# Performance work log

Measured on AMD Instinct MI355X. Metric: run time of the kernel, lower is better.

Reference implementation:

```python
import jax, jax.numpy as jnp
import numpy as np
from jax import lax

B, Cin, C, H, W, Ns, K = 2, 64, 64, 256, 1216, 20000, 9
HW = H * W
D = 2 * C + 3   # 131, MLP input dim
Dh = D // 2     # 65, MLP hidden dim


def _conv(x, w, b, relu):
    y = lax.conv_general_dilated(x, w, (1, 1), 'SAME',
                                 dimension_numbers=('NCHW', 'OIHW', 'NCHW'))
    y = y + b[None, :, None, None]
    return jax.nn.relu(y) if relu else y


def _mlp(f, w1, b1, w2, b2):
    # f: (B, Ns, K, D) -> (B, Ns, K, 1)
    h = jax.nn.leaky_relu(f @ w1 + b1, 0.2)
    return h @ w2 + b2


def setup_inputs() -> dict:
    ks = jax.random.split(jax.random.key(0), 32)
    s = 0.05
    rng = np.random.default_rng(0)
    # unique point indices per batch (torch scatter with dup indices is nondeterministic)
    pc = np.stack([np.sort(rng.choice(HW, Ns, replace=False)) for _ in range(B)])[:, None, :]
    inp = {
        'rgb': jax.random.normal(ks[0], (B, Cin, H, W), jnp.float32),
        'sdepth': jax.random.normal(ks[1], (B, Cin, H, W), jnp.float32),
        'pc_idx': jnp.asarray(pc, dtype=jnp.int32),
        'nbrs_idx': jax.random.randint(ks[2], (B, 1, Ns, K), 0, HW, dtype=jnp.int32),
        'nbrs_disp': jax.random.normal(ks[3], (B, 3, Ns, K), jnp.float32),
        'd_conv0_w': jax.random.normal(ks[4], (C, Cin, 3, 3), jnp.float32) * s,
        'd_conv0_b': jnp.zeros((C,), jnp.float32),
        'd_conv1_w': jax.random.normal(ks[5], (C, Cin, 3, 3), jnp.float32) * s,
        'd_conv1_b': jnp.zeros((C,), jnp.float32),
        'd_conv2_w': jax.random.normal(ks[6], (C, C, 3, 3), jnp.float32) * s,
        'd_conv2_b': jnp.zeros((C,), jnp.float32),
        'r_conv0_w': jax.random.normal(ks[7], (C, Cin, 3, 3), jnp.float32) * s,
        'r_conv0_b': jnp.zeros((C,), jnp.float32),
        'r_conv1_w': jax.random.normal(ks[8], (C, Cin, 3, 3), jnp.float32) * s,
        'r_conv1_b': jnp.zeros((C,), jnp.float32),
        'r_conv2_w': jax.random.normal(ks[9], (C, C, 3, 3), jnp.float32) * s,
        'r_conv2_b': jnp.zeros((C,), jnp.float32),
        'd_w1': jax.random.normal(ks[10], (D, Dh), jnp.float32) * s,
        'd_b1': jnp.zeros((Dh,), jnp.float32),
        'd_w2': jax.random.normal(ks[11], (Dh, 1), jnp.float32) * s,
        'd_b2': jnp.zeros((1,), jnp.float32),
        'r_w1': jax.random.normal(ks[12], (D, Dh), jnp.float32) * s,
        'r_b1': jnp.zeros((Dh,), jnp.float32),
        'r_w2': jax.random.normal(ks[13], (Dh, 1), jnp.float32) * s,
        'r_b2': jnp.zeros((1,), jnp.float32),
        'd_bias': jnp.zeros((C,), jnp.float32),
        'r_bias': jnp.zeros((C,), jnp.float32),
    }
    return inp


def reference(rgb, sdepth, pc_idx, nbrs_idx, nbrs_disp,
              d_conv0_w, d_conv0_b, d_conv1_w, d_conv1_b, d_conv2_w, d_conv2_b,
              r_conv0_w, r_conv0_b, r_conv1_w, r_conv1_b, r_conv2_w, r_conv2_b,
              d_w1, d_b1, d_w2, d_b2, r_w1, r_b1, r_w2, r_b2, d_bias, r_bias):
    d0 = _conv(sdepth, d_conv0_w, d_conv0_b, True)
    d1 = _conv(sdepth, d_conv1_w, d_conv1_b, False)
    r0 = _conv(rgb, r_conv0_w, r_conv0_b, True)
    r1 = _conv(rgb, r_conv1_w, r_conv1_b, False)

    d0f = d0.reshape(B, C, HW)
    r0f = r0.reshape(B, C, HW)

    pcb = jnp.broadcast_to(pc_idx, (B, C, Ns))
    nb = jnp.broadcast_to(nbrs_idx.reshape(B, 1, Ns * K), (B, C, Ns * K))
    d_s = jnp.take_along_axis(d0f, pcb, axis=2)                       # (B,C,Ns)
    d_nn = jnp.take_along_axis(d0f, nb, axis=2).reshape(B, C, Ns, K)  # (B,C,Ns,K)
    r_s = jnp.take_along_axis(r0f, pcb, axis=2)
    # NOTE: faithful to source, r neighbors are gathered from d_feat0
    r_nn = jnp.take_along_axis(d0f, nb, axis=2).reshape(B, C, Ns, K)

    feats = jnp.concatenate([d_nn - d_s[..., None],
                             r_nn - r_s[..., None],
                             nbrs_disp], axis=1)                      # (B,2C+3,Ns,K)
    feats = jnp.moveaxis(feats, 1, -1)                                # (B,Ns,K,2C+3)

    d_attn = jax.nn.softmax(_mlp(feats, d_w1, d_b1, d_w2, d_b2)[..., 0], axis=-1)  # (B,Ns,K)
    r_attn = jax.nn.softmax(_mlp(feats, r_w1, r_b1, r_w2, r_b2)[..., 0], axis=-1)

    d_feat = jnp.einsum('bnk,bcnk->bcn', d_attn, d_nn) + d_bias[None, :, None]
    r_feat = jnp.einsum('bnk,bcnk->bcn', r_attn, r_nn) + r_bias[None, :, None]

    scat = jax.vmap(lambda idx, src: jnp.zeros((C, HW), src.dtype).at[:, idx].set(src))
    d_new = scat(pc_idx[:, 0], d_feat)
    r_new = scat(pc_idx[:, 0], r_feat)

    # mask scatter in source uses index of shape (B,1,Ns): only channel 0 is set
    mask0 = jax.vmap(lambda i: jnp.zeros((HW,), d0f.dtype).at[i].set(1.0))(pc_idx[:, 0])
    masks = jnp.concatenate([mask0[:, None, :], jnp.zeros((B, C - 1, HW), d0f.dtype)], axis=1)

    d0f = (1.0 - masks) * d0f + d_new
    r0f = (1.0 - masks) * r0f + r_new

    d2 = _conv(d0f.reshape(B, C, H, W), d_conv2_w, d_conv2_b, False)
    r2 = _conv(r0f.reshape(B, C, H, W), r_conv2_w, r_conv2_b, False)
    return jax.nn.relu(d2 + d1), jax.nn.relu(r2 + r1)
```

## Files before the change

kernel.cpp:

```cpp
#include <hip/hip_runtime.h>

#define H_ 256
#define W_ 1216
#define HW_ (H_*W_)
#define B_ 2
#define Ns_ 20000
#define K_ 9
#define D_ 131
#define Dh_ 65

#define TPOS 66

typedef __attribute__((ext_vector_type(8))) short bf16x8;
typedef __attribute__((ext_vector_type(4))) float f32x4;

__device__ __forceinline__ float b2f(unsigned short u){
  union { unsigned int i; float f; } v; v.i = ((unsigned int)u) << 16; return v.f;
}
__device__ __forceinline__ unsigned short f2b(float f){
  union { float f; unsigned int i; } v; v.f = f;
  unsigned int r = (v.i + 0x7FFFu + ((v.i >> 16) & 1u)) >> 16;
  return (unsigned short)r;
}

struct WPtrs { const float* w[6]; };

__global__ void prep_w(WPtrs wp, unsigned short* __restrict__ Asw){
  int blk = blockIdx.x;
  int c = blk / 72, rem = blk % 72, mt = rem / 18, kc = rem % 18;
  int lane = threadIdx.x;
  const float* w = wp.w[c];
  int co = mt*16 + (lane & 15);
  int kb = kc*32 + (lane >> 4)*8;
  unsigned short* dst = Asw + ((size_t)blk*64 + lane)*8;
  #pragma unroll
  for (int j = 0; j < 8; ++j){
    int k = kb + j, tap = k >> 6, cin = k & 63;
    dst[j] = f2b(w[((size_t)co*64 + cin)*9 + tap]);
  }
}

__global__ void prep_wmlp(const float* __restrict__ dw1, const float* __restrict__ rw1,
                          unsigned short* __restrict__ Bm){
  int blk = blockIdx.x;
  int nt = blk / 5, ks = blk % 5;
  int lane = threadIdx.x;
  int col = nt*16 + (lane & 15);
  int kb  = ks*32 + (lane >> 4)*8;
  unsigned short* dst = Bm + ((size_t)blk*64 + lane)*8;
  #pragma unroll
  for (int jj = 0; jj < 8; ++jj){
    int row = kb + jj;
    float v = 0.f;
    if (row < D_ && col < 2*Dh_)
      v = (col < Dh_) ? dw1[(size_t)row*Dh_ + col] : rw1[(size_t)row*Dh_ + (col - Dh_)];
    dst[jj] = f2b(v);
  }
}

__global__ __launch_bounds__(256) void transpose_in(
    const float* __restrict__ x, unsigned short* __restrict__ xt)
{
  __shared__ unsigned short t[128*64];
  int tid = threadIdx.x, l = tid & 63, w = tid >> 6;
  int b = blockIdx.y;
  size_t p0 = (size_t)blockIdx.x * 128;
  int pos = (w & 1)*64 + l;
  const float* src = x + (size_t)b*64*HW_ + p0 + pos;
  #pragma unroll
  for (int it = 0; it < 4; ++it){
    int c8 = (w >> 1)*4 + it;
    union { unsigned short us[8]; uint4 v; } pk;
    #pragma unroll
    for (int j = 0; j < 8; ++j)
      pk.us[j] = f2b(src[(size_t)(c8*8 + j)*HW_]);
    *(uint4*)&t[pos*64 + ((c8 ^ (pos & 7)) << 3)] = pk.v;
  }
  __syncthreads();
  unsigned short* dst = xt + ((size_t)b*HW_ + p0)*64;
  #pragma unroll
  for (int it = 0; it < 4; ++it){
    int e = it*256 + tid;
    int pp = e >> 3, sl = e & 7;
    *(uint4*)&dst[(size_t)pp*64 + sl*8] =
        *(const uint4*)&t[pp*64 + ((sl ^ (pp & 7)) << 3)];
  }
}

__global__ __launch_bounds__(256,4) void conv01_mfma(
    const unsigned short* __restrict__ xt,
    const unsigned short* __restrict__ Asw,
    const float* __restrict__ b0, const float* __restrict__ b1,
    unsigned short* __restrict__ y0t, unsigned short* __restrict__ u,
    float* __restrict__ y1out)
{
  __shared__ unsigned short tile[4*TPOS*64];
  int tid = threadIdx.x;
  int c0 = blockIdx.x*64, r0 = blockIdx.y*2, b = blockIdx.z;

  for (int e = tid; e < 4*TPOS*8; e += 256){
    int pos = e >> 3, ch = e & 7;
    int row = pos / TPOS, col = pos - row*TPOS;
    int gy = r0 - 1 + row, gx = c0 - 1 + col;
    uint4 v = {0u,0u,0u,0u};
    if (gy >= 0 && gy < H_ && gx >= 0 && gx < W_)
      v = *(const uint4*)&xt[((size_t)b*HW_ + (size_t)gy*W_ + gx)*64 + ch*8];
    *(uint4*)&tile[pos*64 + ((ch ^ (pos & 7)) << 3)] = v;
  }
  __syncthreads();

  int wave = tid >> 6, lane = tid & 63;
  int quad = lane >> 4, l15 = lane & 15;
  int cobase = (wave & 1)*32;
  int prow = wave >> 1;

  f32x4 acc[2][2][4];
  #pragma unroll
  for (int cv = 0; cv < 2; ++cv)
    #pragma unroll
    for (int mt = 0; mt < 2; ++mt)
      #pragma unroll
      for (int nt = 0; nt < 4; ++nt)
        acc[cv][mt][nt] = (f32x4){0.f,0.f,0.f,0.f};

  const unsigned short* Ap[2][2];
  #pragma unroll
  for (int cv = 0; cv < 2; ++cv)
    #pragma unroll
    for (int mt = 0; mt < 2; ++mt)
      Ap[cv][mt] = Asw + ((size_t)((cv*4 + (wave&1)*2 + mt)*18)*64 + lane)*8;

  #pragma unroll
  for (int tap = 0; tap < 9; ++tap){
    int pbase = (prow + tap/3)*TPOS + l15 + (tap%3);
    int pk = pbase & 7;
    #pragma unroll
    for (int cc = 0; cc < 2; ++cc){
      int kc = tap*2 + cc;
      int sl = ((quad + 4*cc) ^ pk) << 3;
      bf16x8 a[2][2], bb[4];
      #pragma unroll
      for (int cv = 0; cv < 2; ++cv)
        #pragma unroll
        for (int mt = 0; mt < 2; ++mt)
          a[cv][mt] = *(const bf16x8*)(Ap[cv][mt] + (size_t)kc*512);
      #pragma unroll
      for (int nt = 0; nt < 4; ++nt)
        bb[nt] = *(const bf16x8*)&tile[(pbase + nt*16)*64 + sl];
      #pragma unroll
      for (int cv = 0; cv < 2; ++cv)
        #pragma unroll
        for (int mt = 0; mt < 2; ++mt)
          #pragma unroll
          for (int nt = 0; nt < 4; ++nt)
            acc[cv][mt][nt] = __builtin_amdgcn_mfma_f32_16x16x32_bf16(
                a[cv][mt], bb[nt], acc[cv][mt][nt], 0, 0, 0);
    }
  }

  int gy = r0 + prow;
  #pragma unroll
  for (int mt = 0; mt < 2; ++mt){
    int co4 = cobase + mt*16 + quad*4;
    f32x4 bias0 = *(const f32x4*)&b0[co4];
    f32x4 bias1 = *(const f32x4*)&b1[co4];
    #pragma unroll
    for (int nt = 0; nt < 4; ++nt){
      int gx = c0 + nt*16 + l15;
      size_t gpix = (size_t)gy*W_ + gx;
      f32x4 v0 = acc[0][mt][nt] + bias0;
      ushort4 q;
      q.x = f2b(fmaxf(v0.x,0.f)); q.y = f2b(fmaxf(v0.y,0.f));
      q.z = f2b(fmaxf(v0.z,0.f)); q.w = f2b(fmaxf(v0.w,0.f));
      size_t toff = ((size_t)b*HW_ + gpix)*64 + co4;
      *(ushort4*)&y0t[toff] = q;
      *(ushort4*)&u[toff]   = q;
      f32x4 v1 = acc[1][mt][nt] + bias1;
      float* yo = y1out + ((size_t)b*64 + co4)*HW_ + gpix;
      yo[(size_t)0*HW_] = v1.x; yo[(size_t)1*HW_] = v1.y;
      yo[(size_t)2*HW_] = v1.z; yo[(size_t)3*HW_] = v1.w;
    }
  }
}

__global__ __launch_bounds__(256,4) void conv2_mfma(
    const unsigned short* __restrict__ ut,
    const unsigned short* __restrict__ Asw,
    const float* __restrict__ bias,
    float* __restrict__ out)
{
  __shared__ unsigned short tile[4*TPOS*64];
  int tid = threadIdx.x;
  int c0 = blockIdx.x*64, r0 = blockIdx.y*2, b = blockIdx.z;

  for (int e = tid; e < 4*TPOS*8; e += 256){
    int pos = e >> 3, ch = e & 7;
    int row = pos / TPOS, col = pos - row*TPOS;
    int gy = r0 - 1 + row, gx = c0 - 1 + col;
    uint4 v = {0u,0u,0u,0u};
    if (gy >= 0 && gy < H_ && gx >= 0 && gx < W_)
      v = *(const uint4*)&ut[((size_t)b*HW_ + (size_t)gy*W_ + gx)*64 + ch*8];
    *(uint4*)&tile[pos*64 + ((ch ^ (pos & 7)) << 3)] = v;
  }
  __syncthreads();

  int wave = tid >> 6, lane = tid & 63;
  int quad = lane >> 4, l15 = lane & 15;
  int cobase = (wave & 1)*32;
  int prow = wave >> 1;

  f32x4 acc[2][4];
  #pragma unroll
  for (int mt = 0; mt < 2; ++mt)
    #pragma unroll
    for (int nt = 0; nt < 4; ++nt)
      acc[mt][nt] = (f32x4){0.f,0.f,0.f,0.f};

  const unsigned short* Ap[2];
  #pragma unroll
  for (int mt = 0; mt < 2; ++mt)
    Ap[mt] = Asw + ((size_t)(((wave&1)*2 + mt)*18)*64 + lane)*8;

  #pragma unroll
  for (int tap = 0; tap < 9; ++tap){
    int pbase = (prow + tap/3)*TPOS + l15 + (tap%3);
    int pk = pbase & 7;
    #pragma unroll
    for (int cc = 0; cc < 2; ++cc){
      int kc = tap*2 + cc;
      int sl = ((quad + 4*cc) ^ pk) << 3;
      bf16x8 a[2], bb[4];
      #pragma unroll
      for (int mt = 0; mt < 2; ++mt)
        a[mt] = *(const bf16x8*)(Ap[mt] + (size_t)kc*512);
      #pragma unroll
      for (int nt = 0; nt < 4; ++nt)
        bb[nt] = *(const bf16x8*)&tile[(pbase + nt*16)*64 + sl];
      #pragma unroll
      for (int mt = 0; mt < 2; ++mt)
        #pragma unroll
        for (int nt = 0; nt < 4; ++nt)
          acc[mt][nt] = __builtin_amdgcn_mfma_f32_16x16x32_bf16(
              a[mt], bb[nt], acc[mt][nt], 0, 0, 0);
    }
  }

  int gy = r0 + prow;
  #pragma unroll
  for (int mt = 0; mt < 2; ++mt){
    int co4 = cobase + mt*16 + quad*4;
    f32x4 bs = *(const f32x4*)&bias[co4];
    #pragma unroll
    for (int nt = 0; nt < 4; ++nt){
      int gx = c0 + nt*16 + l15;
      size_t gpix = (size_t)gy*W_ + gx;
      float* yo = out + ((size_t)b*64 + co4)*HW_ + gpix;
      f32x4 v = acc[mt][nt] + bs;
      float r0v = v.x + yo[(size_t)0*HW_];
      float r1v = v.y + yo[(size_t)1*HW_];
      float r2v = v.z + yo[(size_t)2*HW_];
      float r3v = v.w + yo[(size_t)3*HW_];
      yo[(size_t)0*HW_] = r0v > 0.f ? r0v : 0.f;
      yo[(size_t)1*HW_] = r1v > 0.f ? r1v : 0.f;
      yo[(size_t)2*HW_] = r2v > 0.f ? r2v : 0.f;
      yo[(size_t)3*HW_] = r3v > 0.f ? r3v : 0.f;
    }
  }
}

#define FBSTR 176

__global__ __launch_bounds__(256) void attn_kernel(
    const unsigned short* __restrict__ d0t, const unsigned short* __restrict__ r0t,
    const int* __restrict__ pc_idx, const int* __restrict__ nbrs_idx,
    const float* __restrict__ disp,
    const unsigned short* __restrict__ Bmlp,
    const float* __restrict__ db2v, const float* __restrict__ dw2,
    const float* __restrict__ rb2v, const float* __restrict__ rw2,
    const float* __restrict__ dbias, const float* __restrict__ rbias,
    unsigned short* __restrict__ u_d, unsigned short* __restrict__ u_r)
{
  __shared__ float feats[9][64];
  __shared__ unsigned short featsB[16][FBSTR];
  __shared__ float ds_s[64], rs_s[64];
  __shared__ float hbuf[2][9][66];
  __shared__ float part2[2][9][8];
  __shared__ float logitS[2][9];
  __shared__ float attnS[2][9];
  __shared__ int nbrS[9];

  int n = blockIdx.x, b = blockIdx.y;
  int tid = threadIdx.x;
  int s = pc_idx[(size_t)b * Ns_ + n];

  {
    uint4 z = {0u,0u,0u,0u};
    uint4* fb = (uint4*)&featsB[0][0];
    for (int e = tid; e < 16*FBSTR/8; e += 256) fb[e] = z;
  }
  if (tid < 9) nbrS[tid] = nbrs_idx[((size_t)b * Ns_ + n) * K_ + tid];
  __syncthreads();

  if (tid < 88){
    int k = tid >> 3, p = tid & 7, c0p = p << 3;
    const unsigned short* srcp =
        (k < 9)  ? &d0t[((size_t)b*HW_ + (size_t)nbrS[k])*64 + c0p] :
        (k == 9) ? &d0t[((size_t)b*HW_ + (size_t)s)*64 + c0p]
                 : &r0t[((size_t)b*HW_ + (size_t)s)*64 + c0p];
    uint4 v = *(const uint4*)srcp;
    const unsigned short* us = (const unsigned short*)&v;
    float* dst = (k < 9) ? &feats[k][c0p] : ((k == 9) ? &ds_s[c0p] : &rs_s[c0p]);
    #pragma unroll
    for (int t2 = 0; t2 < 8; ++t2) dst[t2] = b2f(us[t2]);
  }
  if (tid >= 128 && tid < 155){
    int t2 = tid - 128, m = t2 / 9, k = t2 % 9;
    featsB[k][128 + m] = f2b(disp[(((size_t)b * 3 + m) * Ns_ + n) * K_ + k]);
  }
  __syncthreads();

  for (int e = tid; e < 9*64; e += 256){
    int k = e >> 6, c = e & 63;
    float dnn = feats[k][c];
    featsB[k][c]      = f2b(dnn - ds_s[c]);
    featsB[k][64 + c] = f2b(dnn - rs_s[c]);
  }
  __syncthreads();

  {
    int wave = tid >> 6, lane = tid & 63, quad = lane >> 4, l15 = lane & 15;
    bf16x8 afr[5];
    #pragma unroll
    for (int ks = 0; ks < 5; ++ks)
      afr[ks] = *(const bf16x8*)&featsB[l15][ks*32 + quad*8];
    for (int nt = wave; nt < 9; nt += 4){
      f32x4 acc = (f32x4){0.f,0.f,0.f,0.f};
      const unsigned short* bp = Bmlp + ((size_t)nt*5*64 + lane)*8;
      #pragma unroll
      for (int ks = 0; ks < 5; ++ks){
        bf16x8 bfr = *(const bf16x8*)(bp + (size_t)ks*512);
        acc = __builtin_amdgcn_mfma_f32_16x16x32_bf16(afr[ks], bfr, acc, 0, 0, 0);
      }
      int jq = nt*16 + l15;
      if (jq < 2*Dh_){
        int mlp = (jq >= Dh_) ? 1 : 0;
        int j = jq - mlp*Dh_;
        #pragma unroll
        for (int r = 0; r < 4; ++r){
          int m = quad*4 + r;
          if (m < 9){
            float h = acc[r];
            hbuf[mlp][m][j] = h > 0.f ? h : 0.2f*h;
          }
        }
      }
    }
  }
  __syncthreads();

  if (tid < 144){
    int mlp = tid / 72, r2 = tid % 72, k = r2 >> 3, p = r2 & 7;
    const float* w2 = mlp ? rw2 : dw2;
    float sm = 0.f;
    for (int j = p; j < Dh_; j += 8) sm += hbuf[mlp][k][j] * w2[j];
    part2[mlp][k][p] = sm;
  }
  __syncthreads();

  if (tid < 18){
    int mlp = tid / 9, k = tid % 9;
    float l = (mlp ? rb2v : db2v)[0];
    #pragma unroll
    for (int p = 0; p < 8; ++p) l += part2[mlp][k][p];
    logitS[mlp][k] = l;
  }
  __syncthreads();

  if (tid < 2){
    float m = logitS[tid][0];
    for (int k = 1; k < 9; ++k) m = fmaxf(m, logitS[tid][k]);
    float e[9], sum = 0.f;
    for (int k = 0; k < 9; ++k){ e[k] = __expf(logitS[tid][k] - m); sum += e[k]; }
    float inv = 1.f / sum;
    for (int k = 0; k < 9; ++k) attnS[tid][k] = e[k] * inv;
  }
  __syncthreads();

  if (tid < 128){
    int mlp = tid >> 6, c = tid & 63;
    float f = (mlp ? rbias : dbias)[c];
    #pragma unroll
    for (int k = 0; k < 9; ++k)
      f += attnS[mlp][k] * feats[k][c];
    float base = (c == 0) ? 0.f : (mlp ? rs_s[c] : ds_s[c]);
    unsigned short* u = mlp ? u_r : u_d;
    u[((size_t)b * HW_ + (size_t)s) * 64 + c] = f2b(base + f);
  }
}

extern "C" void kernel_launch(void* const* d_in, const int* in_sizes, int n_in,
                              void* d_out, int out_size, void* d_ws, size_t ws_size,
                              hipStream_t stream)
{
  (void)in_sizes; (void)n_in; (void)out_size; (void)ws_size;

  const float* rgb       = (const float*)d_in[0];
  const float* sdepth    = (const float*)d_in[1];
  const int*   pc_idx    = (const int*)d_in[2];
  const int*   nbrs_idx  = (const int*)d_in[3];
  const float* nbrs_disp = (const float*)d_in[4];

  WPtrs wp;
  wp.w[0] = (const float*)d_in[5];
  wp.w[1] = (const float*)d_in[7];
  wp.w[2] = (const float*)d_in[9];
  wp.w[3] = (const float*)d_in[11];
  wp.w[4] = (const float*)d_in[13];
  wp.w[5] = (const float*)d_in[15];
  const float* d_conv0_b = (const float*)d_in[6];
  const float* d_conv1_b = (const float*)d_in[8];
  const float* d_conv2_b = (const float*)d_in[10];
  const float* r_conv0_b = (const float*)d_in[12];
  const float* r_conv1_b = (const float*)d_in[14];
  const float* r_conv2_b = (const float*)d_in[16];
  const float* d_w1 = (const float*)d_in[17];
  const float* d_w2 = (const float*)d_in[19];
  const float* d_b2 = (const float*)d_in[20];
  const float* r_w1 = (const float*)d_in[21];
  const float* r_w2 = (const float*)d_in[23];
  const float* r_b2 = (const float*)d_in[24];
  const float* d_bias = (const float*)d_in[25];
  const float* r_bias = (const float*)d_in[26];

  char* ws = (char*)d_ws;
  const size_t TSZ = (size_t)B_ * HW_ * 64 * 2;
  unsigned short* u_d = (unsigned short*)(ws + 0*TSZ);
  unsigned short* u_r = (unsigned short*)(ws + 1*TSZ);
  unsigned short* d0t = (unsigned short*)(ws + 2*TSZ);
  unsigned short* r0t = (unsigned short*)(ws + 3*TSZ);
  unsigned short* xt  = (unsigned short*)(ws + 4*TSZ);
  unsigned short* Asw = (unsigned short*)(ws + 5*TSZ);
  const size_t CONV_STRIDE = 4*18*64*8;
  unsigned short* Bmlp = Asw + 6*CONV_STRIDE;

  prep_w<<<432, 64, 0, stream>>>(wp, Asw);
  prep_wmlp<<<45, 64, 0, stream>>>(d_w1, r_w1, Bmlp);

  float* out = (float*)d_out;
  const size_t OUTSZ = (size_t)B_ * 64 * HW_;

  dim3 cgrid(W_/64, H_/2, B_);
  dim3 tgrid(HW_/128, B_);

  transpose_in<<<tgrid, 256, 0, stream>>>(sdepth, xt);
  conv01_mfma<<<cgrid, 256, 0, stream>>>(xt, Asw + 0*CONV_STRIDE,
      d_conv0_b, d_conv1_b, d0t, u_d, out);
  transpose_in<<<tgrid, 256, 0, stream>>>(rgb, xt);
  conv01_mfma<<<cgrid, 256, 0, stream>>>(xt, Asw + 3*CONV_STRIDE,
      r_conv0_b, r_conv1_b, r0t, u_r, out + OUTSZ);

  attn_kernel<<<dim3(Ns_, B_), 256, 0, stream>>>(
      d0t, r0t, pc_idx, nbrs_idx, nbrs_disp,
      Bmlp,
      d_b2, d_w2, r_b2, r_w2,
      d_bias, r_bias,
      u_d, u_r);

  conv2_mfma<<<cgrid, 256, 0, stream>>>(u_d, Asw + 2*CONV_STRIDE, d_conv2_b, out);
  conv2_mfma<<<cgrid, 256, 0, stream>>>(u_r, Asw + 5*CONV_STRIDE, r_conv2_b, out + OUTSZ);
}
```

Before: 1.372 ms.

## Process one point per wave in attention kernel, removing block barriers

Restructures the attention kernel so each 64-lane wave handles one sample point, giving four points per 256-thread block instead of one. Block-wide __syncthreads stages are replaced by per-wave shared memory, shuffle-based index broadcast and reductions. The second MLP layer is fused into the MFMA epilogue, and the softmax is done with wave shuffles instead of shared-memory staging. Each wave now runs all nine MFMA n-tiles itself. There are no barriers between lanes of a wave, so correctness relies on wave-lockstep ordering of the LDS writes and reads.

```diff
diff --git a/kernel.cpp b/kernel.cpp
--- a/kernel.cpp
+++ b/kernel.cpp
@@ -269,6 +269,14 @@
 }
 
 #define FBSTR 176
+#define AW 4
+
+struct __align__(16) WaveShm {
+  unsigned short featsB[16][FBSTR];
+  float feats[9][64];
+  float ds[64], rs[64];
+  float attnw[2][12];
+};
 
 __global__ __launch_bounds__(256) void attn_kernel(
     const unsigned short* __restrict__ d0t, const unsigned short* __restrict__ r0t,
@@ -280,121 +288,169 @@
     const float* __restrict__ dbias, const float* __restrict__ rbias,
     unsigned short* __restrict__ u_d, unsigned short* __restrict__ u_r)
 {
-  __shared__ float feats[9][64];
-  __shared__ unsigned short featsB[16][FBSTR];
-  __shared__ float ds_s[64], rs_s[64];
-  __shared__ float hbuf[2][9][66];
-  __shared__ float part2[2][9][8];
-  __shared__ float logitS[2][9];
-  __shared__ float attnS[2][9];
-  __shared__ int nbrS[9];
-
-  int n = blockIdx.x, b = blockIdx.y;
+  __shared__ WaveShm shm[AW];
   int tid = threadIdx.x;
-  int s = pc_idx[(size_t)b * Ns_ + n];
+  int wave = tid >> 6, lane = tid & 63;
+  int quad = lane >> 4, l15 = lane & 15;
+  int n = blockIdx.x * AW + wave;
+  int b = blockIdx.y;
+  WaveShm& S = shm[wave];
+
+  int s = pc_idx[(size_t)b*Ns_ + n];
+  s = __builtin_amdgcn_readfirstlane(s);
+
+  int myidx = (lane < 9) ? nbrs_idx[((size_t)b*Ns_ + n)*K_ + lane] : 0;
+  int idx8 = __shfl(myidx, 8);
 
   {
     uint4 z = {0u,0u,0u,0u};
-    uint4* fb = (uint4*)&featsB[0][0];
-    for (int e = tid; e < 16*FBSTR/8; e += 256) fb[e] = z;
-  }
-  if (tid < 9) nbrS[tid] = nbrs_idx[((size_t)b * Ns_ + n) * K_ + tid];
-  __syncthreads();
-
-  if (tid < 88){
-    int k = tid >> 3, p = tid & 7, c0p = p << 3;
-    const unsigned short* srcp =
-        (k < 9)  ? &d0t[((size_t)b*HW_ + (size_t)nbrS[k])*64 + c0p] :
-        (k == 9) ? &d0t[((size_t)b*HW_ + (size_t)s)*64 + c0p]
-                 : &r0t[((size_t)b*HW_ + (size_t)s)*64 + c0p];
-    uint4 v = *(const uint4*)srcp;
-    const unsigned short* us = (const unsigned short*)&v;
-    float* dst = (k < 9) ? &feats[k][c0p] : ((k == 9) ? &ds_s[c0p] : &rs_s[c0p]);
-    #pragma unroll
-    for (int t2 = 0; t2 < 8; ++t2) dst[t2] = b2f(us[t2]);
-  }
-  if (tid >= 128 && tid < 155){
-    int t2 = tid - 128, m = t2 / 9, k = t2 % 9;
-    featsB[k][128 + m] = f2b(disp[(((size_t)b * 3 + m) * Ns_ + n) * K_ + k]);
-  }
-  __syncthreads();
-
-  for (int e = tid; e < 9*64; e += 256){
-    int k = e >> 6, c = e & 63;
-    float dnn = feats[k][c];
-    featsB[k][c]      = f2b(dnn - ds_s[c]);
-    featsB[k][64 + c] = f2b(dnn - rs_s[c]);
-  }
-  __syncthreads();
-
+    unsigned short* fb = &S.featsB[0][0];
+    #pragma unroll
+    for (int it = 0; it < 6; ++it){
+      int e = it*64 + lane;
+      if (e < 16*FBSTR/8) *(uint4*)&fb[e*8] = z;
+    }
+  }
+  if (lane < 27){
+    int m = lane / 9, k = lane - m*9;
+    S.featsB[k][128 + m] = f2b(disp[(((size_t)b*3 + m)*Ns_ + n)*K_ + k]);
+  }
+
+  int grow = lane >> 3, gp = lane & 7;
+  int gidx = __shfl(myidx, grow);
+  uint4 g1 = *(const uint4*)&d0t[((size_t)b*HW_ + (size_t)gidx)*64 + gp*8];
+  uint4 g2 = {0u,0u,0u,0u};
+  if (lane < 24){
+    int r2 = 8 + grow;
+    int idx2 = (r2 == 8) ? idx8 : s;
+    const unsigned short* base = (r2 == 10) ? r0t : d0t;
+    g2 = *(const uint4*)&base[((size_t)b*HW_ + (size_t)idx2)*64 + gp*8];
+  }
+
+  float dn[8];
   {
-    int wave = tid >> 6, lane = tid & 63, quad = lane >> 4, l15 = lane & 15;
-    bf16x8 afr[5];
-    #pragma unroll
-    for (int ks = 0; ks < 5; ++ks)
-      afr[ks] = *(const bf16x8*)&featsB[l15][ks*32 + quad*8];
-    for (int nt = wave; nt < 9; nt += 4){
-      f32x4 acc = (f32x4){0.f,0.f,0.f,0.f};
-      const unsigned short* bp = Bmlp + ((size_t)nt*5*64 + lane)*8;
-      #pragma unroll
-      for (int ks = 0; ks < 5; ++ks){
-        bf16x8 bfr = *(const bf16x8*)(bp + (size_t)ks*512);
-        acc = __builtin_amdgcn_mfma_f32_16x16x32_bf16(afr[ks], bfr, acc, 0, 0, 0);
+    const unsigned short* us = (const unsigned short*)&g1;
+    #pragma unroll
+    for (int j = 0; j < 8; ++j){ dn[j] = b2f(us[j]); S.feats[grow][gp*8 + j] = dn[j]; }
+  }
+  if (lane >= 8 && lane < 24){
+    const unsigned short* us = (const unsigned short*)&g2;
+    float* dst = (lane < 16) ? &S.ds[(lane - 8)*8] : &S.rs[(lane - 16)*8];
+    #pragma unroll
+    for (int j = 0; j < 8; ++j) dst[j] = b2f(us[j]);
+  }
+
+  {
+    unsigned short od[8], orr[8];
+    #pragma unroll
+    for (int j = 0; j < 8; ++j){
+      int c = gp*8 + j;
+      od[j]  = f2b(dn[j] - S.ds[c]);
+      orr[j] = f2b(dn[j] - S.rs[c]);
+    }
+    *(uint4*)&S.featsB[grow][gp*8]      = *(uint4*)od;
+    *(uint4*)&S.featsB[grow][64 + gp*8] = *(uint4*)orr;
+  }
+  if (lane < 8){
+    const unsigned short* us = (const unsigned short*)&g2;
+    unsigned short od[8], orr[8];
+    #pragma unroll
+    for (int j = 0; j < 8; ++j){
+      int c = lane*8 + j;
+      float v = b2f(us[j]);
+      S.feats[8][c] = v;
+      od[j]  = f2b(v - S.ds[c]);
+      orr[j] = f2b(v - S.rs[c]);
+    }
+    *(uint4*)&S.featsB[8][lane*8]      = *(uint4*)od;
+    *(uint4*)&S.featsB[8][64 + lane*8] = *(uint4*)orr;
+  }
+
+  bf16x8 afr[5];
+  #pragma unroll
+  for (int ks = 0; ks < 5; ++ks)
+    afr[ks] = *(const bf16x8*)&S.featsB[l15][ks*32 + quad*8];
+
+  float pd[2][4];
+  #pragma unroll
+  for (int m = 0; m < 2; ++m)
+    #pragma unroll
+    for (int r = 0; r < 4; ++r) pd[m][r] = 0.f;
+
+  #pragma unroll
+  for (int nt = 0; nt < 9; ++nt){
+    f32x4 acc = (f32x4){0.f,0.f,0.f,0.f};
+    const unsigned short* bp = Bmlp + ((size_t)nt*5*64 + lane)*8;
+    #pragma unroll
+    for (int ks = 0; ks < 5; ++ks){
+      bf16x8 bfr = *(const bf16x8*)(bp + (size_t)ks*512);
+      acc = __builtin_amdgcn_mfma_f32_16x16x32_bf16(afr[ks], bfr, acc, 0, 0, 0);
+    }
+    int jq = nt*16 + l15;
+    if (jq < 2*Dh_){
+      int mlp = (jq >= Dh_) ? 1 : 0;
+      int j = jq - mlp*Dh_;
+      float w2 = mlp ? rw2[j] : dw2[j];
+      #pragma unroll
+      for (int r = 0; r < 4; ++r){
+        float h = acc[r];
+        h = h > 0.f ? h : 0.2f*h;
+        pd[mlp][r] += h * w2;
       }
-      int jq = nt*16 + l15;
-      if (jq < 2*Dh_){
-        int mlp = (jq >= Dh_) ? 1 : 0;
-        int j = jq - mlp*Dh_;
-        #pragma unroll
-        for (int r = 0; r < 4; ++r){
-          int m = quad*4 + r;
-          if (m < 9){
-            float h = acc[r];
-            hbuf[mlp][m][j] = h > 0.f ? h : 0.2f*h;
-          }
-        }
+    }
+  }
+
+  #pragma unroll
+  for (int mask = 1; mask <= 8; mask <<= 1)
+    #pragma unroll
+    for (int m = 0; m < 2; ++m)
+      #pragma unroll
+      for (int r = 0; r < 4; ++r)
+        pd[m][r] += __shfl_xor(pd[m][r], mask);
+
+  float b2c[2] = { db2v[0], rb2v[0] };
+  #pragma unroll
+  for (int m = 0; m < 2; ++m){
+    float lg[4];
+    float mx = -3.4e38f;
+    #pragma unroll
+    for (int r = 0; r < 4; ++r){
+      lg[r] = pd[m][r] + b2c[m];
+      if (quad*4 + r < 9) mx = fmaxf(mx, lg[r]);
+    }
+    mx = fmaxf(mx, __shfl_xor(mx, 16));
+    mx = fmaxf(mx, __shfl_xor(mx, 32));
+    float ex[4], sum = 0.f;
+    #pragma unroll
+    for (int r = 0; r < 4; ++r){
+      int k = quad*4 + r;
+      ex[r] = (k < 9) ? __expf(lg[r] - mx) : 0.f;
+      sum += ex[r];
+    }
+    sum += __shfl_xor(sum, 16);
+    sum += __shfl_xor(sum, 32);
+    float inv = 1.f / sum;
+    if (l15 == 0){
+      #pragma unroll
+      for (int r = 0; r < 4; ++r){
+        int k = quad*4 + r;
+        if (k < 9) S.attnw[m][k] = ex[r] * inv;
       }
     }
   }
-  __syncthreads();
-
-  if (tid < 144){
-    int mlp = tid / 72, r2 = tid % 72, k = r2 >> 3, p = r2 & 7;
-    const float* w2 = mlp ? rw2 : dw2;
-    float sm = 0.f;
-    for (int j = p; j < Dh_; j += 8) sm += hbuf[mlp][k][j] * w2[j];
-    part2[mlp][k][p] = sm;
-  }
-  __syncthreads();
-
-  if (tid < 18){
-    int mlp = tid / 9, k = tid % 9;
-    float l = (mlp ? rb2v : db2v)[0];
-    #pragma unroll
-    for (int p = 0; p < 8; ++p) l += part2[mlp][k][p];
-    logitS[mlp][k] = l;
-  }
-  __syncthreads();
-
-  if (tid < 2){
-    float m = logitS[tid][0];
-    for (int k = 1; k < 9; ++k) m = fmaxf(m, logitS[tid][k]);
-    float e[9], sum = 0.f;
-    for (int k = 0; k < 9; ++k){ e[k] = __expf(logitS[tid][k] - m); sum += e[k]; }
-    float inv = 1.f / sum;
-    for (int k = 0; k < 9; ++k) attnS[tid][k] = e[k] * inv;
-  }
-  __syncthreads();
-
-  if (tid < 128){
-    int mlp = tid >> 6, c = tid & 63;
-    float f = (mlp ? rbias : dbias)[c];
-    #pragma unroll
-    for (int k = 0; k < 9; ++k)
-      f += attnS[mlp][k] * feats[k][c];
-    float base = (c == 0) ? 0.f : (mlp ? rs_s[c] : ds_s[c]);
-    unsigned short* u = mlp ? u_r : u_d;
-    u[((size_t)b * HW_ + (size_t)s) * 64 + c] = f2b(base + f);
+
+  {
+    int c = lane;
+    #pragma unroll
+    for (int m = 0; m < 2; ++m){
+      float f = (m ? rbias : dbias)[c];
+      #pragma unroll
+      for (int k = 0; k < 9; ++k)
+        f += S.attnw[m][k] * S.feats[k][c];
+      float base = (c == 0) ? 0.f : (m ? S.rs[c] : S.ds[c]);
+      unsigned short* u = m ? u_r : u_d;
+      u[((size_t)b*HW_ + (size_t)s)*64 + c] = f2b(base + f);
+    }
   }
 }
 
@@ -459,7 +515,7 @@
   conv01_mfma<<<cgrid, 256, 0, stream>>>(xt, Asw + 3*CONV_STRIDE,
       r_conv0_b, r_conv1_b, r0t, u_r, out + OUTSZ);
 
-  attn_kernel<<<dim3(Ns_, B_), 256, 0, stream>>>(
+  attn_kernel<<<dim3(Ns_/AW, B_), 256, 0, stream>>>(
       d0t, r0t, pc_idx, nbrs_idx, nbrs_disp,
       Bmlp,
       d_b2, d_w2, r_b2, r_w2,
```

Measured after the change: 1.364 ms. About the same (-0.6%).
